# Performance work log

Measured on AMD Instinct MI355X. Metric: run time of the kernel, lower is better.

## Reference

```python
import jax, jax.numpy as jnp
import numpy as np

B, H, D = 4, 16, 64
CTX, BLK = 3072, 1024
ST, HID = 64, 1024
NUM_RELATIONS = 7
KV = CTX + BLK


def setup_inputs() -> dict:
    key = jax.random.key(0)
    ks = jax.random.split(key, 7)
    return {
        "q": jax.random.normal(ks[0], (B, H, BLK, D), jnp.float32),
        "k": jax.random.normal(ks[1], (B, H, KV, D), jnp.float32),
        "v": jax.random.normal(ks[2], (B, H, KV, D), jnp.float32),
        "block_vertex_ids": jax.random.randint(ks[3], (B, BLK), 0, ST, dtype=jnp.int32),
        "vertex_embedding": jax.random.normal(ks[4], (ST, HID), jnp.float32) * 0.02,
        "relation_bias": jax.random.normal(ks[5], (NUM_RELATIONS, H), jnp.float32) * 0.02,
        "relation_matrix": jax.random.randint(ks[6], (ST, ST), 0, NUM_RELATIONS, dtype=jnp.int32),
        "ctx_len": CTX,
        "block_len": BLK,
    }


def reference(q, k, v, block_vertex_ids, vertex_embedding, relation_bias,
              relation_matrix, ctx_len, block_len):
    # q: [B,H,BLK,D]; k,v: [B,H,CTX+BLK,D]
    st = vertex_embedding.shape[0]
    vid = block_vertex_ids % st                      # [B, BLK] (mod st_size, as in score_mod)
    # get_initial_bias: vertex embedding lookup -> [B, BLK, HID]
    init_bias = vertex_embedding[vid]
    # attention scores
    scale = q.shape[-1] ** -0.5
    scores = jnp.einsum('bhqd,bhkd->bhqk', q, k) * scale   # [B,H,BLK,KV]
    # relational bias only for kv_idx >= ctx_len (blk_idx = kv_idx - ctx_len);
    # for kv_idx < ctx_len the score_mod adds zero.
    rel = relation_matrix[vid[:, :, None], vid[:, None, :]]  # [B, BLK, BLK]
    bias = relation_bias[rel]                                # [B, BLK, BLK, H]
    bias = jnp.transpose(bias, (0, 3, 1, 2))                 # [B, H, BLK(q), BLK(k)]
    scores = scores.at[:, :, :, ctx_len:ctx_len + block_len].add(bias)
    attn = jax.nn.softmax(scores, axis=-1)
    out = jnp.einsum('bhqk,bhkd->bhqd', attn, v)             # [B,H,BLK,D]
    return out, init_bias
```

## Files before the change

### kernel.cpp

```cpp
#include <hip/hip_runtime.h>

#define B_    4
#define H_    16
#define D_    64
#define BLK_  1024
#define CTX_  3072
#define KV_   4096
#define ST_   64
#define HID_  1024
#define NREL_ 7
#define NT_   (KV_ / 64)
#define CTXT_ (CTX_ / 64)

#define LOG2E 1.44269504088896340736f

typedef short  bf16x8_t __attribute__((ext_vector_type(8)));
typedef float  f32x4_t  __attribute__((ext_vector_type(4)));
typedef unsigned int u32x4_t __attribute__((ext_vector_type(4)));

typedef unsigned int uint_as1 __attribute__((address_space(1)));
typedef unsigned int uint_as3 __attribute__((address_space(3)));

__device__ inline void gload16(const void* g, void* l) {
    __builtin_amdgcn_global_load_lds((const uint_as1*)g, (uint_as3*)l, 16, 0, 0);
}

__device__ inline unsigned short f2bf(float f) {
    unsigned int u = __float_as_uint(f);
    u = (u + 0x7FFFu + ((u >> 16) & 1u)) >> 16;
    return (unsigned short)u;
}
__device__ inline float bf2f(unsigned short u) {
    return __uint_as_float(((unsigned int)u) << 16);
}
__device__ inline unsigned int cvtpk(float a, float b) {
    unsigned int r;
    asm("v_cvt_pk_bf16_f32 %0, %1, %2" : "=v"(r) : "v"(a), "v"(b));
    return r;
}

__device__ inline int swz(int row, int col) {
    return row * 64 + (col ^ ((row & 7) << 3));
}

__global__ void prep_kv(const float* __restrict__ kg, const float* __restrict__ vg,
                        unsigned short* __restrict__ kimg, unsigned short* __restrict__ vimg)
{
    __shared__ float tile[64][65];
    const int  gb   = blockIdx.x;
    const bool isV  = gb >= (B_ * H_ * NT_);
    const int  blk  = isV ? gb - B_ * H_ * NT_ : gb;
    const float* src = (isV ? vg : kg) + (size_t)blk * 64 * 64;
    unsigned short* dst = (isV ? vimg : kimg) + (size_t)blk * 4096;

    if (!isV) {
        for (int c = threadIdx.x; c < 512; c += 256) {
            const int row = c >> 3, d0 = (c & 7) << 3;
            const f32x4_t a0 = *(const f32x4_t*)(src + row * 64 + d0);
            const f32x4_t a1 = *(const f32x4_t*)(src + row * 64 + d0 + 4);
            u32x4_t o;
            o[0] = cvtpk(a0[0], a0[1]); o[1] = cvtpk(a0[2], a0[3]);
            o[2] = cvtpk(a1[0], a1[1]); o[3] = cvtpk(a1[2], a1[3]);
            *(u32x4_t*)&dst[swz(row, d0)] = o;
        }
    } else {
        for (int c = threadIdx.x; c < 512; c += 256) {
            const int row = c >> 3, d0 = (c & 7) << 3;
            const f32x4_t a0 = *(const f32x4_t*)(src + row * 64 + d0);
            const f32x4_t a1 = *(const f32x4_t*)(src + row * 64 + d0 + 4);
#pragma unroll
            for (int j = 0; j < 4; ++j) { tile[row][d0 + j] = a0[j]; tile[row][d0 + 4 + j] = a1[j]; }
        }
        __syncthreads();
        for (int c = threadIdx.x; c < 512; c += 256) {
            const int d = c >> 3, k0 = (c & 7) << 3;
            u32x4_t o;
#pragma unroll
            for (int j = 0; j < 4; ++j)
                o[j] = cvtpk(tile[k0 + 2 * j][d], tile[k0 + 2 * j + 1][d]);
            *(u32x4_t*)&dst[swz(d, k0)] = o;
        }
    }
}

__global__ __launch_bounds__(256, 3)
void attn_v4(const float* __restrict__ qg,
             const unsigned short* __restrict__ kimg,
             const unsigned short* __restrict__ vimg,
             const int* __restrict__ bvi,
             const float* __restrict__ rbias, const int* __restrict__ rmat,
             float* __restrict__ outg)
{
    __shared__ __align__(16) unsigned short Kb [2][64 * 64];
    __shared__ __align__(16) unsigned short Vtb[2][64 * 64];
    __shared__ __align__(16) unsigned short Pt[4 * 16 * 64];
    __shared__ unsigned short btab[64 * 64];
    __shared__ unsigned char  vkl8[BLK_];

    const int tid  = threadIdx.x;
    const int w    = tid >> 6;
    const int lane = tid & 63;
    const int lo   = lane & 15;
    const int hi   = lane >> 4;

    const int bid  = blockIdx.x;
    const int xcd  = bid & 7;
    const int slot = bid >> 3;
    const int bh   = (slot >> 4) * 8 + xcd;
    const int qt   = slot & 15;
    const int b    = bh >> 4;
    const int h    = bh & 15;
    const int q0   = qt * 64;

    for (int i = tid; i < 64 * 64; i += 256)
        btab[i] = f2bf(rbias[rmat[i] * H_ + h] * LOG2E);
    for (int i = tid; i < BLK_; i += 256)
        vkl8[i] = (unsigned char)(bvi[b * BLK_ + i] & (ST_ - 1));

    const float* qrow = qg + ((size_t)bh * BLK_ + q0 + w * 16 + lo) * D_;
    bf16x8_t qa[2];
#pragma unroll
    for (int kk = 0; kk < 2; ++kk) {
        const f32x4_t x0 = *(const f32x4_t*)(qrow + kk * 32 + hi * 8);
        const f32x4_t x1 = *(const f32x4_t*)(qrow + kk * 32 + hi * 8 + 4);
#pragma unroll
        for (int j = 0; j < 4; ++j) {
            qa[kk][j]     = (short)f2bf(x0[j] * (0.125f * LOG2E));
            qa[kk][4 + j] = (short)f2bf(x1[j] * (0.125f * LOG2E));
        }
    }

    int viq[4];
#pragma unroll
    for (int r = 0; r < 4; ++r)
        viq[r] = bvi[b * BLK_ + q0 + w * 16 + hi * 4 + r] & (ST_ - 1);

    f32x4_t oacc[4];
#pragma unroll
    for (int blk = 0; blk < 4; ++blk) oacc[blk] = (f32x4_t){0.f, 0.f, 0.f, 0.f};
    float lrow[4] = {0.f, 0.f, 0.f, 0.f};

    const char* kbase = (const char*)(kimg + (size_t)bh * NT_ * 4096);
    const char* vbase = (const char*)(vimg + (size_t)bh * NT_ * 4096);

    auto stage = [&](unsigned short* Kl, unsigned short* Vl, int t) {
        const char* kg16 = kbase + (size_t)t * 8192 + w * 2048 + lane * 16;
        const char* vg16 = vbase + (size_t)t * 8192 + w * 2048 + lane * 16;
        char* kl = (char*)Kl + w * 2048;
        char* vl = (char*)Vl + w * 2048;
        gload16(kg16,        kl);
        gload16(kg16 + 1024, kl + 1024);
        gload16(vg16,        vl);
        gload16(vg16 + 1024, vl + 1024);
    };

    auto compute = [&](const unsigned short* Kl, const unsigned short* Vl, int t) {
        f32x4_t sacc[4];
#pragma unroll
        for (int blk = 0; blk < 4; ++blk) sacc[blk] = (f32x4_t){0.f, 0.f, 0.f, 0.f};
#pragma unroll
        for (int kk = 0; kk < 2; ++kk) {
#pragma unroll
            for (int blk = 0; blk < 4; ++blk) {
                const bf16x8_t kb = *(const bf16x8_t*)&Kl[swz(blk * 16 + lo, kk * 32 + hi * 8)];
                sacc[blk] = __builtin_amdgcn_mfma_f32_16x16x32_bf16(qa[kk], kb, sacc[blk], 0, 0, 0);
            }
        }
        if (t >= CTXT_) {
            const int base = (t - CTXT_) * 64;
#pragma unroll
            for (int blk = 0; blk < 4; ++blk) {
                const int vj = vkl8[base + blk * 16 + lo];
#pragma unroll
                for (int r = 0; r < 4; ++r) sacc[blk][r] += bf2f(btab[viq[r] * 64 + vj]);
            }
        }
        unsigned short* pw = &Pt[w * 1024];
#pragma unroll
        for (int blk = 0; blk < 4; ++blk) {
#pragma unroll
            for (int r = 0; r < 4; ++r) {
                const float p = exp2f(sacc[blk][r]);
                sacc[blk][r] = p;
                lrow[r] += p;
            }
            const int col = blk * 16 + lo;
            const unsigned int p01 = cvtpk(sacc[blk][0], sacc[blk][1]);
            const unsigned int p23 = cvtpk(sacc[blk][2], sacc[blk][3]);
            pw[swz(hi * 4 + 0, col)] = (unsigned short)p01;
            pw[swz(hi * 4 + 1, col)] = (unsigned short)(p01 >> 16);
            pw[swz(hi * 4 + 2, col)] = (unsigned short)p23;
            pw[swz(hi * 4 + 3, col)] = (unsigned short)(p23 >> 16);
        }
#pragma unroll
        for (int kk = 0; kk < 2; ++kk) {
            const bf16x8_t pa = *(const bf16x8_t*)&Pt[w * 1024 + swz(lo, kk * 32 + hi * 8)];
#pragma unroll
            for (int blk = 0; blk < 4; ++blk) {
                const bf16x8_t vb = *(const bf16x8_t*)&Vl[swz(blk * 16 + lo, kk * 32 + hi * 8)];
                oacc[blk] = __builtin_amdgcn_mfma_f32_16x16x32_bf16(pa, vb, oacc[blk], 0, 0, 0);
            }
        }
    };

    stage(Kb[0], Vtb[0], 0);
    __syncthreads();

    for (int i = 0; i < NT_ / 2; ++i) {
        const int t0 = 2 * i, t1 = 2 * i + 1;
        stage(Kb[1], Vtb[1], t1);
        compute(Kb[0], Vtb[0], t0);
        __syncthreads();
        if (t1 + 1 < NT_) stage(Kb[0], Vtb[0], t1 + 1);
        compute(Kb[1], Vtb[1], t1);
        __syncthreads();
    }

#pragma unroll
    for (int off = 1; off < 16; off <<= 1) {
#pragma unroll
        for (int r = 0; r < 4; ++r) lrow[r] += __shfl_xor(lrow[r], off, 64);
    }
    float inv[4];
#pragma unroll
    for (int r = 0; r < 4; ++r) inv[r] = 1.0f / lrow[r];

    float* ob = outg + ((size_t)bh * BLK_ + q0 + w * 16) * D_;
#pragma unroll
    for (int blk = 0; blk < 4; ++blk) {
#pragma unroll
        for (int r = 0; r < 4; ++r)
            ob[(hi * 4 + r) * D_ + blk * 16 + lo] = oacc[blk][r] * inv[r];
    }
}

__global__ __launch_bounds__(256, 3)
void attn_v1(const float* __restrict__ qg, const float* __restrict__ kg,
             const float* __restrict__ vg, const int* __restrict__ bvi,
             const float* __restrict__ rbias, const int* __restrict__ rmat,
             float* __restrict__ outg)
{
    __shared__ __align__(16) unsigned short Kt[64 * 64];
    __shared__ __align__(16) unsigned short Vs[64 * 64];
    __shared__ __align__(16) unsigned short Vt[64 * 64];
    __shared__ __align__(16) unsigned short Pt[4 * 16 * 64];
    __shared__ float btab[64 * 64];
    __shared__ int   vkl[64];

    const int tid  = threadIdx.x;
    const int w    = tid >> 6;
    const int lane = tid & 63;
    const int lo   = lane & 15;
    const int hi   = lane >> 4;

    const int bid  = blockIdx.x;
    const int xcd  = bid & 7;
    const int slot = bid >> 3;
    const int bh   = (slot >> 4) * 8 + xcd;
    const int qt   = slot & 15;
    const int b    = bh >> 4;
    const int h    = bh & 15;
    const int q0   = qt * 64;

    for (int i = tid; i < 64 * 64; i += 256)
        btab[i] = rbias[rmat[i] * H_ + h];

    const float* qrow = qg + ((size_t)bh * BLK_ + q0 + w * 16 + lo) * D_;
    bf16x8_t qa[2];
#pragma unroll
    for (int kk = 0; kk < 2; ++kk) {
        const f32x4_t x0 = *(const f32x4_t*)(qrow + kk * 32 + hi * 8);
        const f32x4_t x1 = *(const f32x4_t*)(qrow + kk * 32 + hi * 8 + 4);
#pragma unroll
        for (int j = 0; j < 4; ++j) {
            qa[kk][j]     = (short)f2bf(x0[j] * 0.125f);
            qa[kk][4 + j] = (short)f2bf(x1[j] * 0.125f);
        }
    }

    int viq[4];
#pragma unroll
    for (int r = 0; r < 4; ++r)
        viq[r] = bvi[b * BLK_ + q0 + w * 16 + hi * 4 + r] & (ST_ - 1);

    f32x4_t oacc[4];
#pragma unroll
    for (int blk = 0; blk < 4; ++blk) oacc[blk] = (f32x4_t){0.f, 0.f, 0.f, 0.f};
    float mrow[4], lrow[4];
#pragma unroll
    for (int r = 0; r < 4; ++r) { mrow[r] = -INFINITY; lrow[r] = 0.f; }

    const size_t kvbase = (size_t)bh * KV_ * D_;

    for (int t = 0; t < NT_; ++t) {
        const int kv0 = t * 64;
        __syncthreads();
#pragma unroll
        for (int c = tid; c < 512; c += 256) {
            const int row = c >> 3, d0 = (c & 7) << 3;
            const float* ksrc = kg + kvbase + (size_t)(kv0 + row) * D_ + d0;
            const float* vsrc = vg + kvbase + (size_t)(kv0 + row) * D_ + d0;
            const f32x4_t a0 = *(const f32x4_t*)ksrc, a1 = *(const f32x4_t*)(ksrc + 4);
            const f32x4_t b0 = *(const f32x4_t*)vsrc, b1 = *(const f32x4_t*)(vsrc + 4);
            bf16x8_t kv8, vv8;
#pragma unroll
            for (int j = 0; j < 4; ++j) {
                kv8[j]     = (short)f2bf(a0[j]); kv8[4 + j] = (short)f2bf(a1[j]);
                vv8[j]     = (short)f2bf(b0[j]); vv8[4 + j] = (short)f2bf(b1[j]);
            }
            *(bf16x8_t*)&Kt[swz(row, d0)] = kv8;
            *(bf16x8_t*)&Vs[swz(row, d0)] = vv8;
        }
        const bool isb = (kv0 >= CTX_);
        if (isb && tid < 64) vkl[tid] = bvi[b * BLK_ + (kv0 - CTX_) + tid] & (ST_ - 1);
        __syncthreads();

#pragma unroll
        for (int c = tid; c < 512; c += 256) {
            const int dcol = c >> 3, kvc = (c & 7) << 3;
            bf16x8_t tv;
#pragma unroll
            for (int j = 0; j < 8; ++j) tv[j] = (short)Vs[swz(kvc + j, dcol)];
            *(bf16x8_t*)&Vt[swz(dcol, kvc)] = tv;
        }

        f32x4_t sacc[4];
#pragma unroll
        for (int blk = 0; blk < 4; ++blk) sacc[blk] = (f32x4_t){0.f, 0.f, 0.f, 0.f};
#pragma unroll
        for (int kk = 0; kk < 2; ++kk) {
#pragma unroll
            for (int blk = 0; blk < 4; ++blk) {
                const bf16x8_t kb = *(const bf16x8_t*)&Kt[swz(blk * 16 + lo, kk * 32 + hi * 8)];
                sacc[blk] = __builtin_amdgcn_mfma_f32_16x16x32_bf16(qa[kk], kb, sacc[blk], 0, 0, 0);
            }
        }
        if (isb) {
#pragma unroll
            for (int blk = 0; blk < 4; ++blk) {
                const int vj = vkl[blk * 16 + lo];
#pragma unroll
                for (int r = 0; r < 4; ++r) sacc[blk][r] += btab[viq[r] * 64 + vj];
            }
        }
        f32x4_t tm = sacc[0];
#pragma unroll
        for (int blk = 1; blk < 4; ++blk)
#pragma unroll
            for (int r = 0; r < 4; ++r) tm[r] = fmaxf(tm[r], sacc[blk][r]);
#pragma unroll
        for (int off = 1; off < 16; off <<= 1) {
#pragma unroll
            for (int r = 0; r < 4; ++r) tm[r] = fmaxf(tm[r], __shfl_xor(tm[r], off, 64));
        }
        float corr[4];
#pragma unroll
        for (int r = 0; r < 4; ++r) {
            const float mn = fmaxf(mrow[r], tm[r]);
            corr[r] = __expf(mrow[r] - mn);
            mrow[r] = mn;
        }
        f32x4_t psum = (f32x4_t){0.f, 0.f, 0.f, 0.f};
#pragma unroll
        for (int blk = 0; blk < 4; ++blk) {
#pragma unroll
            for (int r = 0; r < 4; ++r) {
                const float p = __expf(sacc[blk][r] - mrow[r]);
                sacc[blk][r] = p;
                psum[r] += p;
            }
        }
#pragma unroll
        for (int off = 1; off < 16; off <<= 1) {
#pragma unroll
            for (int r = 0; r < 4; ++r) psum[r] += __shfl_xor(psum[r], off, 64);
        }
#pragma unroll
        for (int r = 0; r < 4; ++r) lrow[r] = lrow[r] * corr[r] + psum[r];
#pragma unroll
        for (int blk = 0; blk < 4; ++blk)
#pragma unroll
            for (int r = 0; r < 4; ++r) oacc[blk][r] *= corr[r];

        unsigned short* pw = &Pt[w * 1024];
#pragma unroll
        for (int blk = 0; blk < 4; ++blk) {
            const int col = blk * 16 + lo;
#pragma unroll
            for (int r = 0; r < 4; ++r)
                pw[swz(hi * 4 + r, col)] = f2bf(sacc[blk][r]);
        }
        __syncthreads();
#pragma unroll
        for (int kk = 0; kk < 2; ++kk) {
            const bf16x8_t pa = *(const bf16x8_t*)&Pt[w * 1024 + swz(lo, kk * 32 + hi * 8)];
#pragma unroll
            for (int blk = 0; blk < 4; ++blk) {
                const bf16x8_t vb = *(const bf16x8_t*)&Vt[swz(blk * 16 + lo, kk * 32 + hi * 8)];
                oacc[blk] = __builtin_amdgcn_mfma_f32_16x16x32_bf16(pa, vb, oacc[blk], 0, 0, 0);
            }
        }
    }

    float* ob = outg + ((size_t)bh * BLK_ + q0 + w * 16) * D_;
#pragma unroll
    for (int blk = 0; blk < 4; ++blk) {
#pragma unroll
        for (int r = 0; r < 4; ++r)
            ob[(hi * 4 + r) * D_ + blk * 16 + lo] = oacc[blk][r] / lrow[r];
    }
}

__global__ void ibias_kernel(const int* __restrict__ bvi,
                             const float* __restrict__ emb,
                             float* __restrict__ out2)
{
    const int bq  = blockIdx.x;
    const int vid = bvi[bq] & (ST_ - 1);
    const f32x4_t* src = (const f32x4_t*)(emb + (size_t)vid * HID_);
    f32x4_t*       dst = (f32x4_t*)(out2 + (size_t)bq * HID_);
    for (int i = threadIdx.x; i < HID_ / 4; i += 256) dst[i] = src[i];
}

extern "C" void kernel_launch(void* const* d_in, const int* in_sizes, int n_in,
                              void* d_out, int out_size, void* d_ws, size_t ws_size,
                              hipStream_t stream)
{
    const float* qg    = (const float*)d_in[0];
    const float* kg    = (const float*)d_in[1];
    const float* vg    = (const float*)d_in[2];
    const int*   bvi   = (const int*)d_in[3];
    const float* emb   = (const float*)d_in[4];
    const float* rbias = (const float*)d_in[5];
    const int*   rmat  = (const int*)d_in[6];

    float* outg = (float*)d_out;
    float* out2 = outg + (size_t)B_ * H_ * BLK_ * D_;

    const size_t img_elems = (size_t)B_ * H_ * KV_ * D_;
    const size_t need      = 2 * img_elems * sizeof(unsigned short);

    if (ws_size >= need) {
        unsigned short* kimg = (unsigned short*)d_ws;
        unsigned short* vimg = kimg + img_elems;
        prep_kv<<<dim3(2 * B_ * H_ * NT_), dim3(256), 0, stream>>>(kg, vg, kimg, vimg);
        attn_v4<<<dim3(B_ * H_ * (BLK_ / 64)), dim3(256), 0, stream>>>(
            qg, kimg, vimg, bvi, rbias, rmat, outg);
    } else {
        attn_v1<<<dim3(B_ * H_ * (BLK_ / 64)), dim3(256), 0, stream>>>(
            qg, kg, vg, bvi, rbias, rmat, outg);
    }
    ibias_kernel<<<dim3(B_ * BLK_), dim3(256), 0, stream>>>(bvi, emb, out2);
}
```

Measured before the change: 327.0 us.

## Process two 16-row query sub-tiles per wave to reuse K/V tiles

Each workgroup now covers 128 query rows instead of 64, with every wave handling two 16-row sub-tiles. Each K and V fragment read from LDS feeds two MFMAs, and each K/V tile loaded from global memory serves twice as many queries. This halves the number of workgroups to 512, so fewer blocks run across the CUs. Register use roughly doubles for the accumulators, which is why launch bounds drop to 2 blocks per CU.

```diff
diff --git a/kernel.cpp b/kernel.cpp
--- a/kernel.cpp
+++ b/kernel.cpp
@@ -83,8 +83,8 @@
     }
 }
 
-__global__ __launch_bounds__(256, 3)
-void attn_v4(const float* __restrict__ qg,
+__global__ __launch_bounds__(256, 2)
+void attn_v5(const float* __restrict__ qg,
              const unsigned short* __restrict__ kimg,
              const unsigned short* __restrict__ vimg,
              const int* __restrict__ bvi,
@@ -93,7 +93,7 @@
 {
     __shared__ __align__(16) unsigned short Kb [2][64 * 64];
     __shared__ __align__(16) unsigned short Vtb[2][64 * 64];
-    __shared__ __align__(16) unsigned short Pt[4 * 16 * 64];
+    __shared__ __align__(16) unsigned short Pt[4 * 2 * 16 * 64];
     __shared__ unsigned short btab[64 * 64];
     __shared__ unsigned char  vkl8[BLK_];
 
@@ -106,39 +106,44 @@
     const int bid  = blockIdx.x;
     const int xcd  = bid & 7;
     const int slot = bid >> 3;
-    const int bh   = (slot >> 4) * 8 + xcd;
-    const int qt   = slot & 15;
+    const int bh   = (slot >> 3) * 8 + xcd;
+    const int qt   = slot & 7;
     const int b    = bh >> 4;
     const int h    = bh & 15;
-    const int q0   = qt * 64;
+    const int q0   = qt * 128;
 
     for (int i = tid; i < 64 * 64; i += 256)
         btab[i] = f2bf(rbias[rmat[i] * H_ + h] * LOG2E);
     for (int i = tid; i < BLK_; i += 256)
         vkl8[i] = (unsigned char)(bvi[b * BLK_ + i] & (ST_ - 1));
 
-    const float* qrow = qg + ((size_t)bh * BLK_ + q0 + w * 16 + lo) * D_;
-    bf16x8_t qa[2];
-#pragma unroll
-    for (int kk = 0; kk < 2; ++kk) {
-        const f32x4_t x0 = *(const f32x4_t*)(qrow + kk * 32 + hi * 8);
-        const f32x4_t x1 = *(const f32x4_t*)(qrow + kk * 32 + hi * 8 + 4);
-#pragma unroll
-        for (int j = 0; j < 4; ++j) {
-            qa[kk][j]     = (short)f2bf(x0[j] * (0.125f * LOG2E));
-            qa[kk][4 + j] = (short)f2bf(x1[j] * (0.125f * LOG2E));
-        }
-    }
-
-    int viq[4];
-#pragma unroll
-    for (int r = 0; r < 4; ++r)
-        viq[r] = bvi[b * BLK_ + q0 + w * 16 + hi * 4 + r] & (ST_ - 1);
-
-    f32x4_t oacc[4];
-#pragma unroll
-    for (int blk = 0; blk < 4; ++blk) oacc[blk] = (f32x4_t){0.f, 0.f, 0.f, 0.f};
-    float lrow[4] = {0.f, 0.f, 0.f, 0.f};
+    bf16x8_t qa[2][2];
+    int viq[2][4];
+#pragma unroll
+    for (int sub = 0; sub < 2; ++sub) {
+        const int row0 = q0 + w * 32 + sub * 16;
+        const float* qrow = qg + ((size_t)bh * BLK_ + row0 + lo) * D_;
+#pragma unroll
+        for (int kk = 0; kk < 2; ++kk) {
+            const f32x4_t x0 = *(const f32x4_t*)(qrow + kk * 32 + hi * 8);
+            const f32x4_t x1 = *(const f32x4_t*)(qrow + kk * 32 + hi * 8 + 4);
+#pragma unroll
+            for (int j = 0; j < 4; ++j) {
+                qa[sub][kk][j]     = (short)f2bf(x0[j] * (0.125f * LOG2E));
+                qa[sub][kk][4 + j] = (short)f2bf(x1[j] * (0.125f * LOG2E));
+            }
+        }
+#pragma unroll
+        for (int r = 0; r < 4; ++r)
+            viq[sub][r] = bvi[b * BLK_ + row0 + hi * 4 + r] & (ST_ - 1);
+    }
+
+    f32x4_t oacc[2][4];
+#pragma unroll
+    for (int sub = 0; sub < 2; ++sub)
+#pragma unroll
+        for (int blk = 0; blk < 4; ++blk) oacc[sub][blk] = (f32x4_t){0.f, 0.f, 0.f, 0.f};
+    float lrow[2][4] = {{0.f, 0.f, 0.f, 0.f}, {0.f, 0.f, 0.f, 0.f}};
 
     const char* kbase = (const char*)(kimg + (size_t)bh * NT_ * 4096);
     const char* vbase = (const char*)(vimg + (size_t)bh * NT_ * 4096);
@@ -155,15 +160,18 @@
     };
 
     auto compute = [&](const unsigned short* Kl, const unsigned short* Vl, int t) {
-        f32x4_t sacc[4];
-#pragma unroll
-        for (int blk = 0; blk < 4; ++blk) sacc[blk] = (f32x4_t){0.f, 0.f, 0.f, 0.f};
+        f32x4_t sacc[2][4];
+#pragma unroll
+        for (int sub = 0; sub < 2; ++sub)
+#pragma unroll
+            for (int blk = 0; blk < 4; ++blk) sacc[sub][blk] = (f32x4_t){0.f, 0.f, 0.f, 0.f};
 #pragma unroll
         for (int kk = 0; kk < 2; ++kk) {
 #pragma unroll
             for (int blk = 0; blk < 4; ++blk) {
                 const bf16x8_t kb = *(const bf16x8_t*)&Kl[swz(blk * 16 + lo, kk * 32 + hi * 8)];
-                sacc[blk] = __builtin_amdgcn_mfma_f32_16x16x32_bf16(qa[kk], kb, sacc[blk], 0, 0, 0);
+                sacc[0][blk] = __builtin_amdgcn_mfma_f32_16x16x32_bf16(qa[0][kk], kb, sacc[0][blk], 0, 0, 0);
+                sacc[1][blk] = __builtin_amdgcn_mfma_f32_16x16x32_bf16(qa[1][kk], kb, sacc[1][blk], 0, 0, 0);
             }
         }
         if (t >= CTXT_) {
@@ -172,33 +180,41 @@
             for (int blk = 0; blk < 4; ++blk) {
                 const int vj = vkl8[base + blk * 16 + lo];
 #pragma unroll
-                for (int r = 0; r < 4; ++r) sacc[blk][r] += bf2f(btab[viq[r] * 64 + vj]);
-            }
-        }
-        unsigned short* pw = &Pt[w * 1024];
-#pragma unroll
-        for (int blk = 0; blk < 4; ++blk) {
-#pragma unroll
-            for (int r = 0; r < 4; ++r) {
-                const float p = exp2f(sacc[blk][r]);
-                sacc[blk][r] = p;
-                lrow[r] += p;
-            }
-            const int col = blk * 16 + lo;
-            const unsigned int p01 = cvtpk(sacc[blk][0], sacc[blk][1]);
-            const unsigned int p23 = cvtpk(sacc[blk][2], sacc[blk][3]);
-            pw[swz(hi * 4 + 0, col)] = (unsigned short)p01;
-            pw[swz(hi * 4 + 1, col)] = (unsigned short)(p01 >> 16);
-            pw[swz(hi * 4 + 2, col)] = (unsigned short)p23;
-            pw[swz(hi * 4 + 3, col)] = (unsigned short)(p23 >> 16);
+                for (int sub = 0; sub < 2; ++sub)
+#pragma unroll
+                    for (int r = 0; r < 4; ++r)
+                        sacc[sub][blk][r] += bf2f(btab[viq[sub][r] * 64 + vj]);
+            }
+        }
+#pragma unroll
+        for (int sub = 0; sub < 2; ++sub) {
+            unsigned short* pw = &Pt[w * 2048 + sub * 1024];
+#pragma unroll
+            for (int blk = 0; blk < 4; ++blk) {
+#pragma unroll
+                for (int r = 0; r < 4; ++r) {
+                    const float p = exp2f(sacc[sub][blk][r]);
+                    sacc[sub][blk][r] = p;
+                    lrow[sub][r] += p;
+                }
+                const int col = blk * 16 + lo;
+                const unsigned int p01 = cvtpk(sacc[sub][blk][0], sacc[sub][blk][1]);
+                const unsigned int p23 = cvtpk(sacc[sub][blk][2], sacc[sub][blk][3]);
+                pw[swz(hi * 4 + 0, col)] = (unsigned short)p01;
+                pw[swz(hi * 4 + 1, col)] = (unsigned short)(p01 >> 16);
+                pw[swz(hi * 4 + 2, col)] = (unsigned short)p23;
+                pw[swz(hi * 4 + 3, col)] = (unsigned short)(p23 >> 16);
+            }
         }
 #pragma unroll
         for (int kk = 0; kk < 2; ++kk) {
-            const bf16x8_t pa = *(const bf16x8_t*)&Pt[w * 1024 + swz(lo, kk * 32 + hi * 8)];
+            const bf16x8_t pa0 = *(const bf16x8_t*)&Pt[w * 2048 +        swz(lo, kk * 32 + hi * 8)];
+            const bf16x8_t pa1 = *(const bf16x8_t*)&Pt[w * 2048 + 1024 + swz(lo, kk * 32 + hi * 8)];
 #pragma unroll
             for (int blk = 0; blk < 4; ++blk) {
                 const bf16x8_t vb = *(const bf16x8_t*)&Vl[swz(blk * 16 + lo, kk * 32 + hi * 8)];
-                oacc[blk] = __builtin_amdgcn_mfma_f32_16x16x32_bf16(pa, vb, oacc[blk], 0, 0, 0);
+                oacc[0][blk] = __builtin_amdgcn_mfma_f32_16x16x32_bf16(pa0, vb, oacc[0][blk], 0, 0, 0);
+                oacc[1][blk] = __builtin_amdgcn_mfma_f32_16x16x32_bf16(pa1, vb, oacc[1][blk], 0, 0, 0);
             }
         }
     };
@@ -217,20 +233,22 @@
     }
 
 #pragma unroll
-    for (int off = 1; off < 16; off <<= 1) {
-#pragma unroll
-        for (int r = 0; r < 4; ++r) lrow[r] += __shfl_xor(lrow[r], off, 64);
-    }
-    float inv[4];
-#pragma unroll
-    for (int r = 0; r < 4; ++r) inv[r] = 1.0f / lrow[r];
-
-    float* ob = outg + ((size_t)bh * BLK_ + q0 + w * 16) * D_;
-#pragma unroll
-    for (int blk = 0; blk < 4; ++blk) {
-#pragma unroll
-        for (int r = 0; r < 4; ++r)
-            ob[(hi * 4 + r) * D_ + blk * 16 + lo] = oacc[blk][r] * inv[r];
+    for (int sub = 0; sub < 2; ++sub) {
+#pragma unroll
+        for (int off = 1; off < 16; off <<= 1) {
+#pragma unroll
+            for (int r = 0; r < 4; ++r) lrow[sub][r] += __shfl_xor(lrow[sub][r], off, 64);
+        }
+        float inv[4];
+#pragma unroll
+        for (int r = 0; r < 4; ++r) inv[r] = 1.0f / lrow[sub][r];
+        float* ob = outg + ((size_t)bh * BLK_ + q0 + w * 32 + sub * 16) * D_;
+#pragma unroll
+        for (int blk = 0; blk < 4; ++blk) {
+#pragma unroll
+            for (int r = 0; r < 4; ++r)
+                ob[(hi * 4 + r) * D_ + blk * 16 + lo] = oacc[sub][blk][r] * inv[r];
+        }
     }
 }
 
@@ -444,7 +462,7 @@
         unsigned short* kimg = (unsigned short*)d_ws;
         unsigned short* vimg = kimg + img_elems;
         prep_kv<<<dim3(2 * B_ * H_ * NT_), dim3(256), 0, stream>>>(kg, vg, kimg, vimg);
-        attn_v4<<<dim3(B_ * H_ * (BLK_ / 64)), dim3(256), 0, stream>>>(
+        attn_v5<<<dim3(B_ * H_ * (BLK_ / 128)), dim3(256), 0, stream>>>(
             qg, kimg, vimg, bvi, rbias, rmat, outg);
     } else {
         attn_v1<<<dim3(B_ * H_ * (BLK_ / 64)), dim3(256), 0, stream>>>(
```

After: 315.2 us. 1.04x faster.
